# Optimization experiments

Measured on AMD Instinct MI355X. Metric: run time of the kernel, lower is better.

## Reference

```python
import jax, jax.numpy as jnp
import numpy as np
import math

B_SZ, T_LEN, DIM = 1, 1024, 1024
D_STATE, EXPAND, NUM_SCALES, CONV_K = 16, 2, 3, 4
D_INNER = EXPAND * DIM
EPS_LOG = 1e-38
LN_EPS = 1e-5


def _causal_dwconv(x, w, b):
    # x: (B,T,D), w: (D,1,K) depthwise, b: (D,). torch Conv1d(pad=K-1)[:, :, :T] == left-pad K-1 (causal).
    y = jax.lax.conv_general_dilated(
        jnp.transpose(x, (0, 2, 1)), w, window_strides=(1,),
        padding=[(CONV_K - 1, 0)], dimension_numbers=('NCH', 'OIH', 'NCH'),
        feature_group_count=w.shape[0])
    return jnp.transpose(y, (0, 2, 1)) + b


def _ssm_core(x, cw, cb, xw, dtw, dtb, Dp):
    # x: (B,T,d_inner)
    xc = jax.nn.silu(_causal_dwconv(x, cw, cb))
    proj = xc @ xw.T                               # (B,T,2*d_state)
    B_ssm, C_ssm = proj[..., :D_STATE], proj[..., D_STATE:]
    dt = jax.nn.softplus(B_ssm @ dtw.T + dtb)      # (B,T,d_inner)
    dt = jax.nn.softplus(dt)                       # selective_scan applies softplus a second time (faithful)
    A = -jnp.arange(1, D_STATE + 1, dtype=xc.dtype)  # (d_state,) == -A_init row, same for every d_inner channel
    dA = jnp.exp(dt[..., None] * A)                # (B,T,d_inner,d_state)
    dBx = dt[..., None] * B_ssm[:, :, None, :] * xc[..., None]
    log_dA = jnp.log(jnp.clip(dA, EPS_LOG))
    log_dBx = jnp.log(jnp.clip(dBx, EPS_LOG))
    # parallel_scan_cpu: h = exp(cumsum(log_dA) + logcumsumexp(log_dBx - cumsum(log_dA)))
    a_star = jnp.cumsum(log_dA, axis=1)
    h = jnp.exp(a_star + jax.lax.cumlogsumexp(log_dBx - a_star, axis=1))
    return jnp.einsum('bts,btds->btd', C_ssm, h) + Dp * xc


def _downsample(x, stride):
    if stride == 1:
        return x
    Bb, T, D = x.shape
    Tt = (T // stride) * stride
    return x[:, :Tt].reshape(Bb, Tt // stride, stride, D).mean(2)


def _upsample(x, T_out):
    # F.interpolate(mode='linear', align_corners=False)
    T_in = x.shape[1]
    if T_in == T_out:
        return x
    scale = T_in / T_out
    pos = jnp.clip((jnp.arange(T_out, dtype=jnp.float32) + 0.5) * scale - 0.5, 0.0, T_in - 1)
    lo = jnp.floor(pos).astype(jnp.int32)
    hi = jnp.minimum(lo + 1, T_in - 1)
    w = (pos - lo.astype(pos.dtype))[None, :, None]
    return x[:, lo] * (1.0 - w) + x[:, hi] * w


def _forward(x, in_proj_w, conv_w, conv_b, xproj_w, dtproj_w, dtproj_b,
             D_param, scale_weights, gate_w1, gate_w2, out_proj_w, ln_g, ln_b):
    residual = x
    xz = x @ in_proj_w.T                           # (B,T,2*d_inner)
    x_in, gate = xz[..., :D_INNER], xz[..., D_INNER:]
    outs = []
    for s in range(NUM_SCALES):
        x_s = _downsample(x_in, 2 ** s)
        y_s = _ssm_core(x_s, conv_w[s], conv_b[s], xproj_w[s], dtproj_w[s], dtproj_b[s], D_param[s])
        outs.append(_upsample(y_s, x.shape[1]))
    w = jax.nn.softmax(scale_weights)
    fused = sum(w[s] * outs[s] for s in range(NUM_SCALES))
    ctx = sum(outs) / NUM_SCALES
    gate_ctx = jax.nn.sigmoid(jax.nn.silu(ctx @ gate_w1.T) @ gate_w2.T)
    out = (fused * gate_ctx) * jax.nn.silu(gate)
    out = out @ out_proj_w.T
    y = out + residual
    mu = y.mean(-1, keepdims=True)
    var = ((y - mu) ** 2).mean(-1, keepdims=True)
    return (y - mu) / jnp.sqrt(var + LN_EPS) * ln_g + ln_b


def setup_inputs() -> dict:
    key = jax.random.key(0)
    ks = jax.random.split(key, 12)
    g = lambda k, shp, s: (jax.random.normal(k, shp, jnp.float32) * s)
    return {
        'x': g(ks[0], (B_SZ, T_LEN, DIM), 1.0),
        'in_proj_w': g(ks[1], (2 * D_INNER, DIM), DIM ** -0.5),
        'conv_w': g(ks[2], (NUM_SCALES, D_INNER, 1, CONV_K), CONV_K ** -0.5),
        'conv_b': g(ks[3], (NUM_SCALES, D_INNER), 0.02),
        'xproj_w': g(ks[4], (NUM_SCALES, 2 * D_STATE, D_INNER), D_INNER ** -0.5),
        'dtproj_w': g(ks[5], (NUM_SCALES, D_INNER, D_STATE), D_STATE ** -0.5),
        'dtproj_b': jax.random.uniform(ks[6], (NUM_SCALES, D_INNER), jnp.float32,
                                       math.log(0.001), math.log(0.1)),
        'D_param': jnp.ones((NUM_SCALES, D_INNER), jnp.float32),
        'scale_weights': jnp.ones((NUM_SCALES,), jnp.float32) / NUM_SCALES,
        'gate_w1': g(ks[7], (D_INNER // 2, D_INNER), D_INNER ** -0.5),
        'gate_w2': g(ks[8], (D_INNER, D_INNER // 2), (D_INNER // 2) ** -0.5),
        'out_proj_w': g(ks[9], (DIM, D_INNER), D_INNER ** -0.5),
        'ln_g': jnp.ones((DIM,), jnp.float32),
        'ln_b': jnp.zeros((DIM,), jnp.float32),
    }


def reference(x, in_proj_w, conv_w, conv_b, xproj_w, dtproj_w, dtproj_b,
              D_param, scale_weights, gate_w1, gate_w2, out_proj_w, ln_g, ln_b):
    return _forward(x, in_proj_w, conv_w, conv_b, xproj_w, dtproj_w, dtproj_b,
                    D_param, scale_weights, gate_w1, gate_w2, out_proj_w, ln_g, ln_b)
```

## Files before the change

kernel.cpp:

```cpp
#include <hip/hip_runtime.h>

typedef unsigned short u16;
typedef float floatx2 __attribute__((ext_vector_type(2)));
typedef float floatx4 __attribute__((ext_vector_type(4)));
typedef short shortx8 __attribute__((ext_vector_type(8)));

#define DIN 2048

__device__ __forceinline__ u16 f2bf(float f){
  unsigned u = __float_as_uint(f);
  u = (u + 0x7fffu + ((u>>16)&1u))>>16;
  return (u16)u;
}
__device__ __forceinline__ float sigf(float x){ return 1.f/(1.f+__expf(-x)); }
__device__ __forceinline__ float siluf(float x){ return x*sigf(x); }
__device__ __forceinline__ floatx2 max2(floatx2 a, floatx2 b){
  floatx2 r; r.x = fmaxf(a.x, b.x); r.y = fmaxf(a.y, b.y); return r;
}

#define OFF_WINP  0ull
#define OFF_WG1   8388608ull
#define OFF_WG2   12582912ull
#define OFF_WOP   16777216ull
#define OFF_XB    20971520ull
#define OFF_XIN   23068672ull
#define OFF_SGATE 31457280ull
#define OFF_X1    39845888ull
#define OFF_X2    44040192ull
#define OFF_XC0   46137344ull
#define OFF_XC1   54525952ull
#define OFF_FUSED 60817408ull
#define OFF_G3O   69206016ull
#define OFF_Y0    75497472ull
#define OFF_Y1    83886080ull
#define OFF_Y2    88080384ull
#define OFF_P0    90177536ull
#define OFF_P1    90308608ull
#define OFF_P2    90374144ull
#define OFF_HC    92274688ull
#define OFF_HINIT 121634816ull
#define OFF_SARR  136314880ull
#define OFF_CTXB  OFF_XC0
#define OFF_T1B   OFF_XC1
#define OFF_T1A0  OFF_XIN
#define OFF_T1A1  OFF_X1
#define OFF_YPA0  OFF_Y1
#define OFF_YPA1  (OFF_XC0 + 4194304ull)

__device__ __forceinline__ void gld_lds16(const void* g, void* l){
  __builtin_amdgcn_global_load_lds((const __attribute__((address_space(1))) unsigned*)g,
                                   (__attribute__((address_space(3))) unsigned*)l, 16, 0, 0);
}

__global__ __launch_bounds__(256) void cvt_kernel(
    const float* __restrict__ s0, u16* __restrict__ d0,
    const float* __restrict__ s1, u16* __restrict__ d1)
{
  int i = (blockIdx.x*256 + threadIdx.x)*4;
  const float* s; u16* d;
  if (i < 4194304){ s=s0; d=d0; }
  else            { s=s1; d=d1; i -= 4194304; }
  const float4 v = *(const float4*)(s + i);
  ushort4 o; o.x = f2bf(v.x); o.y = f2bf(v.y); o.z = f2bf(v.z); o.w = f2bf(v.w);
  *(ushort4*)(d + i) = o;
}

template<int MODE, int BM>
__global__ __launch_bounds__(256) void gemm_bt(
    const u16* __restrict__ A, const u16* __restrict__ B,
    int N, int K, int Ks,
    float* __restrict__ out_f, float* __restrict__ out_f2, u16* __restrict__ out_b,
    const float* __restrict__ ex0f, const float* __restrict__ ex1f,
    float* __restrict__ ex0, float* __restrict__ ex1)
{
  constexpr int NI = BM/32;
  constexpr int IP = BM/64;
  __shared__ u16 smA[2][BM*32];
  __shared__ u16 smB[2][BM*32];
  const int tid  = threadIdx.x;
  const int m0   = blockIdx.y * BM;
  const int n0   = blockIdx.x * BM;
  const int wv   = tid >> 6;
  const int lane = tid & 63;
  const int mw   = (wv >> 1) * (BM/2);
  const int nw   = (wv & 1) * (BM/2);
  const int quad = lane >> 4;
  const int l16  = lane & 15;
  const int srow = tid >> 2;
  const int scol = (tid & 3) * 8;

  floatx4 acc[NI][NI];
#pragma unroll
  for (int i=0;i<NI;i++)
#pragma unroll
    for (int j=0;j<NI;j++) acc[i][j] = (floatx4)0.f;

  const int kStart = blockIdx.z * Ks;
  const int kEnd   = kStart + Ks;

  auto stage = [&](int buf, int k0){
#pragma unroll
    for (int p=0;p<IP;p++){
      gld_lds16(A + (size_t)(m0 + p*64 + srow)*K + k0 + scol, &smA[buf][p*2048 + wv*512]);
      gld_lds16(B + (size_t)(n0 + p*64 + srow)*K + k0 + scol, &smB[buf][p*2048 + wv*512]);
    }
  };

  stage(0, kStart);
  int cur = 0;
  for (int k0 = kStart; k0 < kEnd; k0 += 32) {
    __syncthreads();
    if (k0 + 32 < kEnd) stage(cur^1, k0+32);
    shortx8 af[NI], bfr[NI];
#pragma unroll
    for (int i=0;i<NI;i++){
      af[i]  = *(const shortx8*)&smA[cur][(mw + i*16 + l16)*32 + quad*8];
      bfr[i] = *(const shortx8*)&smB[cur][(nw + i*16 + l16)*32 + quad*8];
    }
#pragma unroll
    for (int i=0;i<NI;i++)
#pragma unroll
      for (int j=0;j<NI;j++)
        acc[i][j] = __builtin_amdgcn_mfma_f32_16x16x32_bf16(af[i], bfr[j], acc[i][j], 0, 0, 0);
    cur ^= 1;
  }

#pragma unroll
  for (int i=0;i<NI;i++){
    const int mb = m0 + mw + i*16 + quad*4;
#pragma unroll
    for (int j=0;j<NI;j++){
      const int n = n0 + nw + j*16 + l16;
      const floatx4 v4 = acc[i][j];
      if (MODE == 0){
        if (n < 2048){
#pragma unroll
          for (int r=0;r<4;r++) out_f[(size_t)(mb+r)*2048 + n] = v4[r];
          ex0[(size_t)(mb>>1)*2048 + n]       = 0.5f*(v4[0]+v4[1]);
          ex0[(size_t)((mb>>1)+1)*2048 + n]   = 0.5f*(v4[2]+v4[3]);
          ex1[(size_t)(mb>>2)*2048 + n]       = 0.25f*(v4[0]+v4[1]+v4[2]+v4[3]);
        } else {
#pragma unroll
          for (int r=0;r<4;r++) out_f2[(size_t)(mb+r)*2048 + (n-2048)] = siluf(v4[r]);
        }
      } else if (MODE == 2){
#pragma unroll
        for (int r=0;r<4;r++){
          const size_t idx = (size_t)(mb+r)*N + n;
          out_b[idx] = f2bf(sigf(v4[r]) * ex0f[idx] * ex1f[idx]);
        }
      } else {
        float* dst = blockIdx.z ? out_f2 : out_f;
#pragma unroll
        for (int r=0;r<4;r++) dst[(size_t)(mb+r)*N + n] = v4[r];
      }
    }
  }
}

__global__ __launch_bounds__(256) void g2_epi(const float* __restrict__ a,
    const float* __restrict__ b, u16* __restrict__ o){
  const int i = (blockIdx.x*256 + threadIdx.x)*4;
  const float4 va = *(const float4*)(a+i);
  const float4 vb = *(const float4*)(b+i);
  ushort4 r;
  r.x = f2bf(siluf(va.x+vb.x)); r.y = f2bf(siluf(va.y+vb.y));
  r.z = f2bf(siluf(va.z+vb.z)); r.w = f2bf(siluf(va.w+vb.w));
  *(ushort4*)(o+i) = r;
}

__global__ __launch_bounds__(256) void xproj_kernel(const float* __restrict__ x0,
    const float* __restrict__ x1, const float* __restrict__ x2,
    const float* __restrict__ cw, const float* __restrict__ cb,
    const float* __restrict__ xw,
    float* __restrict__ p0, float* __restrict__ p1, float* __restrict__ p2,
    const float* __restrict__ gw1c, u16* __restrict__ wG1o,
    const float* __restrict__ gw2c, u16* __restrict__ wG2o,
    const float* __restrict__ opwc, u16* __restrict__ wOpo){
  __shared__ float srow[DIN];
  if (blockIdx.x >= 1792){
    int i = (int)(blockIdx.x - 1792)*1024 + threadIdx.x*4;
    const float* sp; u16* dp;
    if (i < 2097152)      { sp=gw1c; dp=wG1o; }
    else if (i < 4194304) { sp=gw2c; dp=wG2o; i-=2097152; }
    else                  { sp=opwc; dp=wOpo; i-=4194304; }
    const float4 v = *(const float4*)(sp + i);
    ushort4 o; o.x = f2bf(v.x); o.y = f2bf(v.y); o.z = f2bf(v.z); o.w = f2bf(v.w);
    *(ushort4*)(dp + i) = o;
    return;
  }
  const int b = blockIdx.x;
  const float* xs; float* proj; int s, t;
  if (b < 1024)      { s=0; t=b;       xs=x0; proj=p0; }
  else if (b < 1536) { s=1; t=b-1024;  xs=x1; proj=p1; }
  else               { s=2; t=b-1536;  xs=x2; proj=p2; }
  const int tid = threadIdx.x;
#pragma unroll
  for (int q=0;q<2;q++){
    const int k = (q*256 + tid)*4;
    float4 xv[4];
#pragma unroll
    for (int j=0;j<4;j++){
      const int tt = t - 3 + j;
      if (tt >= 0) xv[j] = *(const float4*)(xs + (size_t)tt*DIN + k);
      else { xv[j].x = 0.f; xv[j].y = 0.f; xv[j].z = 0.f; xv[j].w = 0.f; }
    }
    const float4 w0 = *(const float4*)(cw + ((size_t)(s*DIN) + k + 0)*4);
    const float4 w1 = *(const float4*)(cw + ((size_t)(s*DIN) + k + 1)*4);
    const float4 w2 = *(const float4*)(cw + ((size_t)(s*DIN) + k + 2)*4);
    const float4 w3 = *(const float4*)(cw + ((size_t)(s*DIN) + k + 3)*4);
    const float4 cb4 = *(const float4*)(cb + (size_t)(s*DIN) + k);
    float4 r;
    r.x = siluf(cb4.x + w0.x*xv[0].x + w0.y*xv[1].x + w0.z*xv[2].x + w0.w*xv[3].x);
    r.y = siluf(cb4.y + w1.x*xv[0].y + w1.y*xv[1].y + w1.z*xv[2].y + w1.w*xv[3].y);
    r.z = siluf(cb4.z + w2.x*xv[0].z + w2.y*xv[1].z + w2.z*xv[2].z + w2.w*xv[3].z);
    r.w = siluf(cb4.w + w3.x*xv[0].w + w3.y*xv[1].w + w3.z*xv[2].w + w3.w*xv[3].w);
    *(float4*)&srow[k] = r;
  }
  __syncthreads();
  const int i = tid >> 3;
  const int j = tid & 7;
  const float4* w4 = (const float4*)(xw + ((size_t)s*32 + i)*DIN);
  const float4* s4 = (const float4*)srow;
  float acc = 0.f;
#pragma unroll 8
  for (int c=0;c<64;c++){
    const float4 sv = s4[j + 8*c];
    const float4 wv = w4[j + 8*c];
    acc += sv.x*wv.x + sv.y*wv.y + sv.z*wv.z + sv.w*wv.w;
  }
  acc += __shfl_xor(acc,1); acc += __shfl_xor(acc,2); acc += __shfl_xor(acc,4);
  if (j == 0) proj[t*32 + i] = acc;
}

__global__ __launch_bounds__(128) void scan_p1(
    const float* __restrict__ x0, const float* __restrict__ x1, const float* __restrict__ x2,
    const float* __restrict__ p0, const float* __restrict__ p1, const float* __restrict__ p2,
    const float* __restrict__ cw, const float* __restrict__ cb,
    const float* __restrict__ dtw, const float* __restrict__ dtb,
    float* __restrict__ Sarr, float* __restrict__ Hc)
{
  __shared__ float sproj[16*32];
  int b = blockIdx.x;
  const float *xs, *proj; int base, s;
  if (b < 1024)      { xs=x0; proj=p0; base=0;  s=0; }
  else if (b < 1536) { b-=1024; xs=x1; proj=p1; base=64; s=1; }
  else               { b-=1536; xs=x2; proj=p2; base=96; s=2; }
  const int chunk = b >> 4;
  const int tid   = threadIdx.x;
  const int d     = (b & 15)*128 + tid;
  const int t0    = chunk*16;
  {
    const int k = tid*4;
    *(float4*)&sproj[k] = *(const float4*)&proj[t0*32 + k];
  }
  __syncthreads();

  const float4 wc  = *(const float4*)(cw + ((size_t)(s*DIN) + d)*4);
  const float  cbv = cb[s*DIN + d];
  floatx2 w2[8];
  const floatx2* wr = (const floatx2*)(dtw + ((size_t)(s*DIN) + d)*16);
#pragma unroll
  for (int k=0;k<8;k++) w2[k] = wr[k];
  const float bias = dtb[s*DIN + d];
  const floatx2 eps2 = {1e-38f, 1e-38f};

  floatx2 H2[8];
#pragma unroll
  for (int k=0;k<8;k++) H2[k] = (floatx2)0.f;
  float S = 0.f;
  const float* xp = xs + d;
  float h0=0.f, h1=0.f, h2=0.f;
  if (chunk){
    h0 = xp[(size_t)(t0-3)*DIN];
    h1 = xp[(size_t)(t0-2)*DIN];
    h2 = xp[(size_t)(t0-1)*DIN];
  }
  for (int tt=0; tt<16; tt++){
    const float xv  = xp[(size_t)(t0+tt)*DIN];
    const float xcv = siluf(cbv + wc.x*h0 + wc.y*h1 + wc.z*h2 + wc.w*xv);
    h0=h1; h1=h2; h2=xv;
    const floatx2* Bp2 = (const floatx2*)&sproj[tt*32];
    floatx2 zz = (floatx2)0.f;
#pragma unroll
    for (int k=0;k<8;k++) zz += Bp2[k]*w2[k];
    float z = fminf(zz.x + zz.y + bias, 60.f);
    const float E     = __expf(z);
    const float denom = 2.f + E;
    const float e     = __builtin_amdgcn_rcpf(denom);
    const float dtv   = __logf(denom);
    S += dtv;
    const floatx2 c2  = {dtv*xcv, dtv*xcv};
    const floatx2 es  = {e*e, e*e};
    floatx2 ep2 = {e, e*e};
#pragma unroll
    for (int k=0;k<8;k++){
      const floatx2 dA  = max2(ep2, eps2);
      const floatx2 dBx = max2(c2*Bp2[k], eps2);
      H2[k] = dA*H2[k] + dBx;
      ep2 *= es;
    }
  }
  Sarr[(size_t)(base+chunk)*2048 + d] = S;
  float* o = Hc + (size_t)(base+chunk)*32768 + d;
#pragma unroll
  for (int k=0;k<8;k++){
    o[(size_t)(2*k  )*2048] = H2[k].x;
    o[(size_t)(2*k+1)*2048] = H2[k].y;
  }
}

__global__ __launch_bounds__(256) void scan_combine(const float* __restrict__ Sarr,
    const float* __restrict__ Hc, float* __restrict__ Hinit){
  int id = blockIdx.x*256 + threadIdx.x;
  int base, C;
  if (id < 32768)      { base=0;  C=64; }
  else if (id < 65536) { id-=32768; base=64; C=32; }
  else                 { id-=65536; base=96; C=16; }
  const int n = id >> 11, d = id & 2047;
  const float fn = -(float)(n+1);
  const size_t off = (size_t)base*32768 + id;
  const float* hc = Hc + off;
  float* hi = Hinit + off;
  const float* sp = Sarr + (size_t)base*2048 + d;
  float H = 0.f;
  for (int c=0;c<C;c++){
    hi[(size_t)c*32768] = H;
    const float e = __expf(fn * sp[(size_t)c*2048]);
    H = e*H + hc[(size_t)c*32768];
  }
}

__global__ __launch_bounds__(128) void scan_p2(
    const float* __restrict__ x0, const float* __restrict__ x1, const float* __restrict__ x2,
    const float* __restrict__ p0, const float* __restrict__ p1, const float* __restrict__ p2,
    const float* __restrict__ cw, const float* __restrict__ cb,
    const float* __restrict__ dtw, const float* __restrict__ dtb,
    const float* __restrict__ Hinit, const float* __restrict__ Dp_all,
    float* __restrict__ y0, float* __restrict__ y1, float* __restrict__ y2)
{
  __shared__ float sproj[16*32];
  int b = blockIdx.x;
  const float *xs, *proj; float* y; int base, s;
  if (b < 1024)      { xs=x0; proj=p0; y=y0; base=0;  s=0; }
  else if (b < 1536) { b-=1024; xs=x1; proj=p1; y=y1; base=64; s=1; }
  else               { b-=1536; xs=x2; proj=p2; y=y2; base=96; s=2; }
  const int chunk = b >> 4;
  const int tid   = threadIdx.x;
  const int d     = (b & 15)*128 + tid;
  const int t0    = chunk*16;
  {
    const int k = tid*4;
    *(float4*)&sproj[k] = *(const float4*)&proj[t0*32 + k];
  }
  __syncthreads();

  const float4 wc  = *(const float4*)(cw + ((size_t)(s*DIN) + d)*4);
  const float  cbv = cb[s*DIN + d];
  floatx2 w2[8];
  const floatx2* wr = (const floatx2*)(dtw + ((size_t)(s*DIN) + d)*16);
#pragma unroll
  for (int k=0;k<8;k++) w2[k] = wr[k];
  const float bias = dtb[s*DIN + d];

  floatx2 H2[8];
  const float* hi = Hinit + (size_t)(base+chunk)*32768 + d;
#pragma unroll
  for (int k=0;k<8;k++){
    H2[k].x = hi[(size_t)(2*k  )*2048];
    H2[k].y = hi[(size_t)(2*k+1)*2048];
  }
  const float Dv = Dp_all[s*DIN + d];
  const floatx2 eps2 = {1e-38f, 1e-38f};
  const float* xp = xs + d;
  float* yp = y + (size_t)t0*DIN + d;
  float h0=0.f, h1=0.f, h2=0.f;
  if (chunk){
    h0 = xp[(size_t)(t0-3)*DIN];
    h1 = xp[(size_t)(t0-2)*DIN];
    h2 = xp[(size_t)(t0-1)*DIN];
  }
  for (int tt=0; tt<16; tt++){
    const float xv  = xp[(size_t)(t0+tt)*DIN];
    const float xcv = siluf(cbv + wc.x*h0 + wc.y*h1 + wc.z*h2 + wc.w*xv);
    h0=h1; h1=h2; h2=xv;
    const floatx2* Bp2 = (const floatx2*)&sproj[tt*32];
    floatx2 zz = (floatx2)0.f;
#pragma unroll
    for (int k=0;k<8;k++) zz += Bp2[k]*w2[k];
    float z = fminf(zz.x + zz.y + bias, 60.f);
    const float E     = __expf(z);
    const float denom = 2.f + E;
    const float e     = __builtin_amdgcn_rcpf(denom);
    const float dtv   = __logf(denom);
    const floatx2 c2 = {dtv*xcv, dtv*xcv};
    const floatx2 es = {e*e, e*e};
    floatx2 ep2 = {e, e*e};
    floatx2 pacc2 = (floatx2)0.f;
#pragma unroll
    for (int k=0;k<8;k++){
      const floatx2 dA  = max2(ep2, eps2);
      const floatx2 dBx = max2(c2*Bp2[k], eps2);
      H2[k] = dA*H2[k] + dBx;
      pacc2 += Bp2[8+k]*H2[k];
      ep2 *= es;
    }
    yp[(size_t)tt*DIN] = pacc2.x + pacc2.y + Dv*xcv;
  }
}

__device__ __forceinline__ float ups_read(const float* __restrict__ ys, int Tin, int t, int d){
  const float scale = (float)Tin * (1.f/1024.f);
  float pos = ((float)t + 0.5f)*scale - 0.5f;
  pos = fminf(fmaxf(pos, 0.f), (float)(Tin-1));
  const int lo = (int)floorf(pos);
  const float w = pos - (float)lo;
  const int hi = min(lo+1, Tin-1);
  return ys[(size_t)lo*DIN + d]*(1.f-w) + ys[(size_t)hi*DIN + d]*w;
}

__global__ __launch_bounds__(256) void fuse_kernel(const float* __restrict__ y0,
    const float* __restrict__ y1, const float* __restrict__ y2,
    const float* __restrict__ sw, u16* __restrict__ ctxb, float* __restrict__ fused){
  const int idx = blockIdx.x*256 + threadIdx.x;
  const int t = idx >> 11, d = idx & 2047;
  const float w0r = sw[0], w1r = sw[1], w2r = sw[2];
  const float mx = fmaxf(w0r, fmaxf(w1r, w2r));
  float e0 = __expf(w0r-mx), e1 = __expf(w1r-mx), e2 = __expf(w2r-mx);
  const float inv = 1.f/(e0+e1+e2);
  e0 *= inv; e1 *= inv; e2 *= inv;
  const float o0 = y0[idx];
  const float o1 = ups_read(y1, 512, t, d);
  const float o2 = ups_read(y2, 256, t, d);
  fused[idx] = e0*o0 + e1*o1 + e2*o2;
  ctxb[idx]  = f2bf((o0+o1+o2)*(1.f/3.f));
}

__global__ __launch_bounds__(256) void ln_kernel(const float* __restrict__ ya,
    const float* __restrict__ yb, const float* __restrict__ xr,
    const float* __restrict__ g, const float* __restrict__ b, float* __restrict__ out){
  __shared__ float red[4];
  const int t = blockIdx.x;
  const size_t ro = (size_t)t*1024;
  float v[4];
  float s = 0.f;
#pragma unroll
  for (int i=0;i<4;i++){
    const int c = threadIdx.x + i*256;
    v[i] = ya[ro+c] + yb[ro+c] + xr[ro+c];
    s += v[i];
  }
  s += __shfl_xor(s,1); s += __shfl_xor(s,2); s += __shfl_xor(s,4);
  s += __shfl_xor(s,8); s += __shfl_xor(s,16); s += __shfl_xor(s,32);
  if ((threadIdx.x & 63) == 0) red[threadIdx.x>>6] = s;
  __syncthreads();
  const float mu = (red[0]+red[1]+red[2]+red[3]) * (1.f/1024.f);
  __syncthreads();
  float q = 0.f;
#pragma unroll
  for (int i=0;i<4;i++){ const float dd = v[i]-mu; q += dd*dd; }
  q += __shfl_xor(q,1); q += __shfl_xor(q,2); q += __shfl_xor(q,4);
  q += __shfl_xor(q,8); q += __shfl_xor(q,16); q += __shfl_xor(q,32);
  if ((threadIdx.x & 63) == 0) red[threadIdx.x>>6] = q;
  __syncthreads();
  const float rstd = rsqrtf((red[0]+red[1]+red[2]+red[3]) * (1.f/1024.f) + 1e-5f);
#pragma unroll
  for (int i=0;i<4;i++){
    const int c = threadIdx.x + i*256;
    out[ro + c] = (v[i]-mu)*rstd*g[c] + b[c];
  }
}

extern "C" void kernel_launch(void* const* d_in, const int* in_sizes, int n_in,
                              void* d_out, int out_size, void* d_ws, size_t ws_size,
                              hipStream_t stream) {
  const float* x     = (const float*)d_in[0];
  const float* inpw  = (const float*)d_in[1];
  const float* convw = (const float*)d_in[2];
  const float* convb = (const float*)d_in[3];
  const float* xpw   = (const float*)d_in[4];
  const float* dtw   = (const float*)d_in[5];
  const float* dtb   = (const float*)d_in[6];
  const float* Dp    = (const float*)d_in[7];
  const float* sw    = (const float*)d_in[8];
  const float* gw1   = (const float*)d_in[9];
  const float* gw2   = (const float*)d_in[10];
  const float* opw   = (const float*)d_in[11];
  const float* lng   = (const float*)d_in[12];
  const float* lnb   = (const float*)d_in[13];
  float* out = (float*)d_out;

  char* ws = (char*)d_ws;
  u16*    wInp  = (u16*)   (ws + OFF_WINP);
  u16*    wG1   = (u16*)   (ws + OFF_WG1);
  u16*    wG2   = (u16*)   (ws + OFF_WG2);
  u16*    wOp   = (u16*)   (ws + OFF_WOP);
  u16*    xb    = (u16*)   (ws + OFF_XB);
  float*  xin   = (float*) (ws + OFF_XIN);
  float*  sgate = (float*) (ws + OFF_SGATE);
  float*  x1    = (float*) (ws + OFF_X1);
  float*  x2    = (float*) (ws + OFF_X2);
  float*  y0    = (float*) (ws + OFF_Y0);
  float*  y1    = (float*) (ws + OFF_Y1);
  float*  y2    = (float*) (ws + OFF_Y2);
  float*  p0    = (float*) (ws + OFF_P0);
  float*  p1    = (float*) (ws + OFF_P1);
  float*  p2    = (float*) (ws + OFF_P2);
  float*  Sarr  = (float*) (ws + OFF_SARR);
  float*  Hc    = (float*) (ws + OFF_HC);
  float*  Hinit = (float*) (ws + OFF_HINIT);
  u16*    ctxb  = (u16*)   (ws + OFF_CTXB);
  u16*    t1b   = (u16*)   (ws + OFF_T1B);
  float*  fused = (float*) (ws + OFF_FUSED);
  u16*    g3o   = (u16*)   (ws + OFF_G3O);
  float*  t1a0  = (float*) (ws + OFF_T1A0);
  float*  t1a1  = (float*) (ws + OFF_T1A1);
  float*  ypa0  = (float*) (ws + OFF_YPA0);
  float*  ypa1  = (float*) (ws + OFF_YPA1);

  cvt_kernel<<<5120, 256, 0, stream>>>(inpw, wInp, x, xb);
  gemm_bt<0,64><<<dim3(64, 16, 1), 256, 0, stream>>>(xb, wInp, 4096, 1024, 1024,
                                                     xin, sgate, nullptr, nullptr, nullptr, x1, x2);
  xproj_kernel<<<7936, 256, 0, stream>>>(xin, x1, x2, convw, convb, xpw, p0, p1, p2,
                                         gw1, wG1, gw2, wG2, opw, wOp);
  scan_p1<<<1792, 128, 0, stream>>>(xin, x1, x2, p0, p1, p2, convw, convb, dtw, dtb, Sarr, Hc);
  scan_combine<<<384, 256, 0, stream>>>(Sarr, Hc, Hinit);
  scan_p2<<<1792, 128, 0, stream>>>(xin, x1, x2, p0, p1, p2, convw, convb, dtw, dtb,
                                    Hinit, Dp, y0, y1, y2);
  fuse_kernel<<<(1024*DIN)/256, 256, 0, stream>>>(y0, y1, y2, sw, ctxb, fused);
  gemm_bt<4,64><<<dim3(16, 16, 2), 256, 0, stream>>>(ctxb, wG1, 1024, 2048, 1024,
                                                     t1a0, t1a1, nullptr, nullptr, nullptr, nullptr, nullptr);
  g2_epi<<<1024, 256, 0, stream>>>(t1a0, t1a1, t1b);
  gemm_bt<2,64><<<dim3(32, 16, 1), 256, 0, stream>>>(t1b, wG2, 2048, 1024, 1024,
                                                     nullptr, nullptr, g3o, fused, sgate, nullptr, nullptr);
  gemm_bt<4,64><<<dim3(16, 16, 2), 256, 0, stream>>>(g3o, wOp, 1024, 2048, 1024,
                                                     ypa0, ypa1, nullptr, nullptr, nullptr, nullptr, nullptr);
  ln_kernel<<<1024, 256, 0, stream>>>(ypa0, ypa1, x, lng, lnb, out);
}
```

Baseline: 280.3 us.

## Fuse scan passes, combine and scale fusion into one persistent kernel with grid barriers

```diff
diff --git a/kernel.cpp b/kernel.cpp
--- a/kernel.cpp
+++ b/kernel.cpp
@@ -40,6 +40,7 @@
 #define OFF_HC    92274688ull
 #define OFF_HINIT 121634816ull
 #define OFF_SARR  136314880ull
+#define OFF_BAR   137232384ull
 #define OFF_CTXB  OFF_XC0
 #define OFF_T1B   OFF_XC1
 #define OFF_T1A0  OFF_XIN
@@ -52,10 +53,23 @@
                                    (__attribute__((address_space(3))) unsigned*)l, 16, 0, 0);
 }
 
+__device__ __forceinline__ void gbar(unsigned* cnt, unsigned expected){
+  __syncthreads();
+  if (threadIdx.x == 0){
+    __threadfence();
+    atomicAdd(cnt, 1u);
+    while (atomicAdd(cnt, 0u) < expected) __builtin_amdgcn_s_sleep(16);
+    __threadfence();
+  }
+  __syncthreads();
+}
+
 __global__ __launch_bounds__(256) void cvt_kernel(
     const float* __restrict__ s0, u16* __restrict__ d0,
-    const float* __restrict__ s1, u16* __restrict__ d1)
+    const float* __restrict__ s1, u16* __restrict__ d1,
+    unsigned* __restrict__ bar)
 {
+  if (blockIdx.x == 0 && threadIdx.x < 4) bar[threadIdx.x] = 0u;
   int i = (blockIdx.x*256 + threadIdx.x)*4;
   const float* s; u16* d;
   if (i < 4194304){ s=s0; d=d0; }
@@ -233,182 +247,6 @@
   if (j == 0) proj[t*32 + i] = acc;
 }
 
-__global__ __launch_bounds__(128) void scan_p1(
-    const float* __restrict__ x0, const float* __restrict__ x1, const float* __restrict__ x2,
-    const float* __restrict__ p0, const float* __restrict__ p1, const float* __restrict__ p2,
-    const float* __restrict__ cw, const float* __restrict__ cb,
-    const float* __restrict__ dtw, const float* __restrict__ dtb,
-    float* __restrict__ Sarr, float* __restrict__ Hc)
-{
-  __shared__ float sproj[16*32];
-  int b = blockIdx.x;
-  const float *xs, *proj; int base, s;
-  if (b < 1024)      { xs=x0; proj=p0; base=0;  s=0; }
-  else if (b < 1536) { b-=1024; xs=x1; proj=p1; base=64; s=1; }
-  else               { b-=1536; xs=x2; proj=p2; base=96; s=2; }
-  const int chunk = b >> 4;
-  const int tid   = threadIdx.x;
-  const int d     = (b & 15)*128 + tid;
-  const int t0    = chunk*16;
-  {
-    const int k = tid*4;
-    *(float4*)&sproj[k] = *(const float4*)&proj[t0*32 + k];
-  }
-  __syncthreads();
-
-  const float4 wc  = *(const float4*)(cw + ((size_t)(s*DIN) + d)*4);
-  const float  cbv = cb[s*DIN + d];
-  floatx2 w2[8];
-  const floatx2* wr = (const floatx2*)(dtw + ((size_t)(s*DIN) + d)*16);
-#pragma unroll
-  for (int k=0;k<8;k++) w2[k] = wr[k];
-  const float bias = dtb[s*DIN + d];
-  const floatx2 eps2 = {1e-38f, 1e-38f};
-
-  floatx2 H2[8];
-#pragma unroll
-  for (int k=0;k<8;k++) H2[k] = (floatx2)0.f;
-  float S = 0.f;
-  const float* xp = xs + d;
-  float h0=0.f, h1=0.f, h2=0.f;
-  if (chunk){
-    h0 = xp[(size_t)(t0-3)*DIN];
-    h1 = xp[(size_t)(t0-2)*DIN];
-    h2 = xp[(size_t)(t0-1)*DIN];
-  }
-  for (int tt=0; tt<16; tt++){
-    const float xv  = xp[(size_t)(t0+tt)*DIN];
-    const float xcv = siluf(cbv + wc.x*h0 + wc.y*h1 + wc.z*h2 + wc.w*xv);
-    h0=h1; h1=h2; h2=xv;
-    const floatx2* Bp2 = (const floatx2*)&sproj[tt*32];
-    floatx2 zz = (floatx2)0.f;
-#pragma unroll
-    for (int k=0;k<8;k++) zz += Bp2[k]*w2[k];
-    float z = fminf(zz.x + zz.y + bias, 60.f);
-    const float E     = __expf(z);
-    const float denom = 2.f + E;
-    const float e     = __builtin_amdgcn_rcpf(denom);
-    const float dtv   = __logf(denom);
-    S += dtv;
-    const floatx2 c2  = {dtv*xcv, dtv*xcv};
-    const floatx2 es  = {e*e, e*e};
-    floatx2 ep2 = {e, e*e};
-#pragma unroll
-    for (int k=0;k<8;k++){
-      const floatx2 dA  = max2(ep2, eps2);
-      const floatx2 dBx = max2(c2*Bp2[k], eps2);
-      H2[k] = dA*H2[k] + dBx;
-      ep2 *= es;
-    }
-  }
-  Sarr[(size_t)(base+chunk)*2048 + d] = S;
-  float* o = Hc + (size_t)(base+chunk)*32768 + d;
-#pragma unroll
-  for (int k=0;k<8;k++){
-    o[(size_t)(2*k  )*2048] = H2[k].x;
-    o[(size_t)(2*k+1)*2048] = H2[k].y;
-  }
-}
-
-__global__ __launch_bounds__(256) void scan_combine(const float* __restrict__ Sarr,
-    const float* __restrict__ Hc, float* __restrict__ Hinit){
-  int id = blockIdx.x*256 + threadIdx.x;
-  int base, C;
-  if (id < 32768)      { base=0;  C=64; }
-  else if (id < 65536) { id-=32768; base=64; C=32; }
-  else                 { id-=65536; base=96; C=16; }
-  const int n = id >> 11, d = id & 2047;
-  const float fn = -(float)(n+1);
-  const size_t off = (size_t)base*32768 + id;
-  const float* hc = Hc + off;
-  float* hi = Hinit + off;
-  const float* sp = Sarr + (size_t)base*2048 + d;
-  float H = 0.f;
-  for (int c=0;c<C;c++){
-    hi[(size_t)c*32768] = H;
-    const float e = __expf(fn * sp[(size_t)c*2048]);
-    H = e*H + hc[(size_t)c*32768];
-  }
-}
-
-__global__ __launch_bounds__(128) void scan_p2(
-    const float* __restrict__ x0, const float* __restrict__ x1, const float* __restrict__ x2,
-    const float* __restrict__ p0, const float* __restrict__ p1, const float* __restrict__ p2,
-    const float* __restrict__ cw, const float* __restrict__ cb,
-    const float* __restrict__ dtw, const float* __restrict__ dtb,
-    const float* __restrict__ Hinit, const float* __restrict__ Dp_all,
-    float* __restrict__ y0, float* __restrict__ y1, float* __restrict__ y2)
-{
-  __shared__ float sproj[16*32];
-  int b = blockIdx.x;
-  const float *xs, *proj; float* y; int base, s;
-  if (b < 1024)      { xs=x0; proj=p0; y=y0; base=0;  s=0; }
-  else if (b < 1536) { b-=1024; xs=x1; proj=p1; y=y1; base=64; s=1; }
-  else               { b-=1536; xs=x2; proj=p2; y=y2; base=96; s=2; }
-  const int chunk = b >> 4;
-  const int tid   = threadIdx.x;
-  const int d     = (b & 15)*128 + tid;
-  const int t0    = chunk*16;
-  {
-    const int k = tid*4;
-    *(float4*)&sproj[k] = *(const float4*)&proj[t0*32 + k];
-  }
-  __syncthreads();
-
-  const float4 wc  = *(const float4*)(cw + ((size_t)(s*DIN) + d)*4);
-  const float  cbv = cb[s*DIN + d];
-  floatx2 w2[8];
-  const floatx2* wr = (const floatx2*)(dtw + ((size_t)(s*DIN) + d)*16);
-#pragma unroll
-  for (int k=0;k<8;k++) w2[k] = wr[k];
-  const float bias = dtb[s*DIN + d];
-
-  floatx2 H2[8];
-  const float* hi = Hinit + (size_t)(base+chunk)*32768 + d;
-#pragma unroll
-  for (int k=0;k<8;k++){
-    H2[k].x = hi[(size_t)(2*k  )*2048];
-    H2[k].y = hi[(size_t)(2*k+1)*2048];
-  }
-  const float Dv = Dp_all[s*DIN + d];
-  const floatx2 eps2 = {1e-38f, 1e-38f};
-  const float* xp = xs + d;
-  float* yp = y + (size_t)t0*DIN + d;
-  float h0=0.f, h1=0.f, h2=0.f;
-  if (chunk){
-    h0 = xp[(size_t)(t0-3)*DIN];
-    h1 = xp[(size_t)(t0-2)*DIN];
-    h2 = xp[(size_t)(t0-1)*DIN];
-  }
-  for (int tt=0; tt<16; tt++){
-    const float xv  = xp[(size_t)(t0+tt)*DIN];
-    const float xcv = siluf(cbv + wc.x*h0 + wc.y*h1 + wc.z*h2 + wc.w*xv);
-    h0=h1; h1=h2; h2=xv;
-    const floatx2* Bp2 = (const floatx2*)&sproj[tt*32];
-    floatx2 zz = (floatx2)0.f;
-#pragma unroll
-    for (int k=0;k<8;k++) zz += Bp2[k]*w2[k];
-    float z = fminf(zz.x + zz.y + bias, 60.f);
-    const float E     = __expf(z);
-    const float denom = 2.f + E;
-    const float e     = __builtin_amdgcn_rcpf(denom);
-    const float dtv   = __logf(denom);
-    const floatx2 c2 = {dtv*xcv, dtv*xcv};
-    const floatx2 es = {e*e, e*e};
-    floatx2 ep2 = {e, e*e};
-    floatx2 pacc2 = (floatx2)0.f;
-#pragma unroll
-    for (int k=0;k<8;k++){
-      const floatx2 dA  = max2(ep2, eps2);
-      const floatx2 dBx = max2(c2*Bp2[k], eps2);
-      H2[k] = dA*H2[k] + dBx;
-      pacc2 += Bp2[8+k]*H2[k];
-      ep2 *= es;
-    }
-    yp[(size_t)tt*DIN] = pacc2.x + pacc2.y + Dv*xcv;
-  }
-}
-
 __device__ __forceinline__ float ups_read(const float* __restrict__ ys, int Tin, int t, int d){
   const float scale = (float)Tin * (1.f/1024.f);
   float pos = ((float)t + 0.5f)*scale - 0.5f;
@@ -419,21 +257,166 @@
   return ys[(size_t)lo*DIN + d]*(1.f-w) + ys[(size_t)hi*DIN + d]*w;
 }
 
-__global__ __launch_bounds__(256) void fuse_kernel(const float* __restrict__ y0,
-    const float* __restrict__ y1, const float* __restrict__ y2,
-    const float* __restrict__ sw, u16* __restrict__ ctxb, float* __restrict__ fused){
-  const int idx = blockIdx.x*256 + threadIdx.x;
-  const int t = idx >> 11, d = idx & 2047;
-  const float w0r = sw[0], w1r = sw[1], w2r = sw[2];
-  const float mx = fmaxf(w0r, fmaxf(w1r, w2r));
-  float e0 = __expf(w0r-mx), e1 = __expf(w1r-mx), e2 = __expf(w2r-mx);
-  const float inv = 1.f/(e0+e1+e2);
-  e0 *= inv; e1 *= inv; e2 *= inv;
-  const float o0 = y0[idx];
-  const float o1 = ups_read(y1, 512, t, d);
-  const float o2 = ups_read(y2, 256, t, d);
-  fused[idx] = e0*o0 + e1*o1 + e2*o2;
-  ctxb[idx]  = f2bf((o0+o1+o2)*(1.f/3.f));
+__global__ __launch_bounds__(256, 4) void scan_fused(
+    const float* __restrict__ x0, const float* __restrict__ x1, const float* __restrict__ x2,
+    const float* __restrict__ p0, const float* __restrict__ p1, const float* __restrict__ p2,
+    const float* __restrict__ cw, const float* __restrict__ cb,
+    const float* __restrict__ dtw, const float* __restrict__ dtb,
+    const float* __restrict__ Dp_all, const float* __restrict__ sw,
+    float* __restrict__ Sarr, float* __restrict__ Hc, float* __restrict__ Hinit,
+    float* __restrict__ y0, float* __restrict__ y1, float* __restrict__ y2,
+    u16* __restrict__ ctxb, float* __restrict__ fusedo, unsigned* bar)
+{
+  __shared__ float sproj[16*32];
+  int b = blockIdx.x;
+  const float *xs, *proj; float* y; int base, s;
+  if (b < 512)      { xs=x0; proj=p0; y=y0; base=0;  s=0; }
+  else if (b < 768) { b-=512; xs=x1; proj=p1; y=y1; base=64; s=1; }
+  else              { b-=768; xs=x2; proj=p2; y=y2; base=96; s=2; }
+  const int chunk = b >> 3;
+  const int tid   = threadIdx.x;
+  const int d     = (b & 7)*256 + tid;
+  const int t0    = chunk*16;
+  {
+    const int k = tid*2;
+    *(float2*)&sproj[k] = *(const float2*)&proj[t0*32 + k];
+  }
+  __syncthreads();
+
+  const float4 wc  = *(const float4*)(cw + ((size_t)(s*DIN) + d)*4);
+  const float  cbv = cb[s*DIN + d];
+  floatx2 w2[8];
+  const floatx2* wr = (const floatx2*)(dtw + ((size_t)(s*DIN) + d)*16);
+#pragma unroll
+  for (int k=0;k<8;k++) w2[k] = wr[k];
+  const float bias = dtb[s*DIN + d];
+  const floatx2 eps2 = {1e-38f, 1e-38f};
+
+  floatx2 H2[8];
+#pragma unroll
+  for (int k=0;k<8;k++) H2[k] = (floatx2)0.f;
+  float S = 0.f;
+  float dt_s[16], xcv_s[16];
+  const float* xp = xs + d;
+  float h0=0.f, h1=0.f, h2=0.f;
+  if (chunk){
+    h0 = xp[(size_t)(t0-3)*DIN];
+    h1 = xp[(size_t)(t0-2)*DIN];
+    h2 = xp[(size_t)(t0-1)*DIN];
+  }
+#pragma unroll
+  for (int tt=0; tt<16; tt++){
+    const float xv  = xp[(size_t)(t0+tt)*DIN];
+    const float xcv = siluf(cbv + wc.x*h0 + wc.y*h1 + wc.z*h2 + wc.w*xv);
+    h0=h1; h1=h2; h2=xv;
+    const floatx2* Bp2 = (const floatx2*)&sproj[tt*32];
+    floatx2 zz = (floatx2)0.f;
+#pragma unroll
+    for (int k=0;k<8;k++) zz += Bp2[k]*w2[k];
+    float z = fminf(zz.x + zz.y + bias, 60.f);
+    const float E     = __expf(z);
+    const float denom = 2.f + E;
+    const float e     = __builtin_amdgcn_rcpf(denom);
+    const float dtv   = __logf(denom);
+    dt_s[tt]  = dtv;
+    xcv_s[tt] = xcv;
+    S += dtv;
+    const floatx2 c2  = {dtv*xcv, dtv*xcv};
+    const floatx2 es  = {e*e, e*e};
+    floatx2 ep2 = {e, e*e};
+#pragma unroll
+    for (int k=0;k<8;k++){
+      const floatx2 dA  = max2(ep2, eps2);
+      const floatx2 dBx = max2(c2*Bp2[k], eps2);
+      H2[k] = dA*H2[k] + dBx;
+      ep2 *= es;
+    }
+  }
+  Sarr[(size_t)(base+chunk)*2048 + d] = S;
+  {
+    float* o = Hc + (size_t)(base+chunk)*32768 + d;
+#pragma unroll
+    for (int k=0;k<8;k++){
+      o[(size_t)(2*k  )*2048] = H2[k].x;
+      o[(size_t)(2*k+1)*2048] = H2[k].y;
+    }
+  }
+
+  gbar(bar+0, 896);
+
+  {
+    int id = blockIdx.x*256 + tid;
+    if (id < 98304){
+      int base2, C;
+      if (id < 32768)      { base2=0;  C=64; }
+      else if (id < 65536) { id-=32768; base2=64; C=32; }
+      else                 { id-=65536; base2=96; C=16; }
+      const int n = id >> 11, dd = id & 2047;
+      const float fn = -(float)(n+1);
+      const size_t off = (size_t)base2*32768 + id;
+      const float* hc = Hc + off;
+      float* hi = Hinit + off;
+      const float* sp = Sarr + (size_t)base2*2048 + dd;
+      float H = 0.f;
+      for (int c=0;c<C;c++){
+        hi[(size_t)c*32768] = H;
+        const float e = __expf(fn * sp[(size_t)c*2048]);
+        H = e*H + hc[(size_t)c*32768];
+      }
+    }
+  }
+
+  gbar(bar+1, 896);
+
+  {
+    const float* hi = Hinit + (size_t)(base+chunk)*32768 + d;
+#pragma unroll
+    for (int k=0;k<8;k++){
+      H2[k].x = hi[(size_t)(2*k  )*2048];
+      H2[k].y = hi[(size_t)(2*k+1)*2048];
+    }
+  }
+  const float Dv = Dp_all[s*DIN + d];
+  float* yp = y + (size_t)t0*DIN + d;
+#pragma unroll
+  for (int tt=0; tt<16; tt++){
+    const float dtv = dt_s[tt];
+    const float xcv = xcv_s[tt];
+    const float e   = __expf(-dtv);
+    const floatx2* Bp2 = (const floatx2*)&sproj[tt*32];
+    const floatx2 c2 = {dtv*xcv, dtv*xcv};
+    const floatx2 es = {e*e, e*e};
+    floatx2 ep2 = {e, e*e};
+    floatx2 pacc2 = (floatx2)0.f;
+#pragma unroll
+    for (int k=0;k<8;k++){
+      const floatx2 dA  = max2(ep2, eps2);
+      const floatx2 dBx = max2(c2*Bp2[k], eps2);
+      H2[k] = dA*H2[k] + dBx;
+      pacc2 += Bp2[8+k]*H2[k];
+      ep2 *= es;
+    }
+    yp[(size_t)tt*DIN] = pacc2.x + pacc2.y + Dv*xcv;
+  }
+
+  gbar(bar+2, 896);
+
+  {
+    const float w0r = sw[0], w1r = sw[1], w2r = sw[2];
+    const float mx = fmaxf(w0r, fmaxf(w1r, w2r));
+    float e0 = __expf(w0r-mx), e1 = __expf(w1r-mx), e2 = __expf(w2r-mx);
+    const float inv = 1.f/(e0+e1+e2);
+    e0 *= inv; e1 *= inv; e2 *= inv;
+    const int gid = blockIdx.x*256 + tid;
+    for (int idx = gid; idx < 1024*2048; idx += 896*256){
+      const int t = idx >> 11, dd = idx & 2047;
+      const float o0 = y0[idx];
+      const float o1 = ups_read(y1, 512, t, dd);
+      const float o2 = ups_read(y2, 256, t, dd);
+      fusedo[idx] = e0*o0 + e1*o1 + e2*o2;
+      ctxb[idx]   = f2bf((o0+o1+o2)*(1.f/3.f));
+    }
+  }
 }
 
 __global__ __launch_bounds__(256) void ln_kernel(const float* __restrict__ ya,
@@ -491,43 +474,42 @@
   float* out = (float*)d_out;
 
   char* ws = (char*)d_ws;
-  u16*    wInp  = (u16*)   (ws + OFF_WINP);
-  u16*    wG1   = (u16*)   (ws + OFF_WG1);
-  u16*    wG2   = (u16*)   (ws + OFF_WG2);
-  u16*    wOp   = (u16*)   (ws + OFF_WOP);
-  u16*    xb    = (u16*)   (ws + OFF_XB);
-  float*  xin   = (float*) (ws + OFF_XIN);
-  float*  sgate = (float*) (ws + OFF_SGATE);
-  float*  x1    = (float*) (ws + OFF_X1);
-  float*  x2    = (float*) (ws + OFF_X2);
-  float*  y0    = (float*) (ws + OFF_Y0);
-  float*  y1    = (float*) (ws + OFF_Y1);
-  float*  y2    = (float*) (ws + OFF_Y2);
-  float*  p0    = (float*) (ws + OFF_P0);
-  float*  p1    = (float*) (ws + OFF_P1);
-  float*  p2    = (float*) (ws + OFF_P2);
-  float*  Sarr  = (float*) (ws + OFF_SARR);
-  float*  Hc    = (float*) (ws + OFF_HC);
-  float*  Hinit = (float*) (ws + OFF_HINIT);
-  u16*    ctxb  = (u16*)   (ws + OFF_CTXB);
-  u16*    t1b   = (u16*)   (ws + OFF_T1B);
-  float*  fused = (float*) (ws + OFF_FUSED);
-  u16*    g3o   = (u16*)   (ws + OFF_G3O);
-  float*  t1a0  = (float*) (ws + OFF_T1A0);
-  float*  t1a1  = (float*) (ws + OFF_T1A1);
-  float*  ypa0  = (float*) (ws + OFF_YPA0);
-  float*  ypa1  = (float*) (ws + OFF_YPA1);
-
-  cvt_kernel<<<5120, 256, 0, stream>>>(inpw, wInp, x, xb);
+  u16*      wInp  = (u16*)     (ws + OFF_WINP);
+  u16*      wG1   = (u16*)     (ws + OFF_WG1);
+  u16*      wG2   = (u16*)     (ws + OFF_WG2);
+  u16*      wOp   = (u16*)     (ws + OFF_WOP);
+  u16*      xb    = (u16*)     (ws + OFF_XB);
+  float*    xin   = (float*)   (ws + OFF_XIN);
+  float*    sgate = (float*)   (ws + OFF_SGATE);
+  float*    x1    = (float*)   (ws + OFF_X1);
+  float*    x2    = (float*)   (ws + OFF_X2);
+  float*    y0    = (float*)   (ws + OFF_Y0);
+  float*    y1    = (float*)   (ws + OFF_Y1);
+  float*    y2    = (float*)   (ws + OFF_Y2);
+  float*    p0    = (float*)   (ws + OFF_P0);
+  float*    p1    = (float*)   (ws + OFF_P1);
+  float*    p2    = (float*)   (ws + OFF_P2);
+  float*    Sarr  = (float*)   (ws + OFF_SARR);
+  float*    Hc    = (float*)   (ws + OFF_HC);
+  float*    Hinit = (float*)   (ws + OFF_HINIT);
+  u16*      ctxb  = (u16*)     (ws + OFF_CTXB);
+  u16*      t1b   = (u16*)     (ws + OFF_T1B);
+  float*    fused = (float*)   (ws + OFF_FUSED);
+  u16*      g3o   = (u16*)     (ws + OFF_G3O);
+  float*    t1a0  = (float*)   (ws + OFF_T1A0);
+  float*    t1a1  = (float*)   (ws + OFF_T1A1);
+  float*    ypa0  = (float*)   (ws + OFF_YPA0);
+  float*    ypa1  = (float*)   (ws + OFF_YPA1);
+  unsigned* bar   = (unsigned*)(ws + OFF_BAR);
+
+  cvt_kernel<<<5120, 256, 0, stream>>>(inpw, wInp, x, xb, bar);
   gemm_bt<0,64><<<dim3(64, 16, 1), 256, 0, stream>>>(xb, wInp, 4096, 1024, 1024,
                                                      xin, sgate, nullptr, nullptr, nullptr, x1, x2);
   xproj_kernel<<<7936, 256, 0, stream>>>(xin, x1, x2, convw, convb, xpw, p0, p1, p2,
                                          gw1, wG1, gw2, wG2, opw, wOp);
-  scan_p1<<<1792, 128, 0, stream>>>(xin, x1, x2, p0, p1, p2, convw, convb, dtw, dtb, Sarr, Hc);
-  scan_combine<<<384, 256, 0, stream>>>(Sarr, Hc, Hinit);
-  scan_p2<<<1792, 128, 0, stream>>>(xin, x1, x2, p0, p1, p2, convw, convb, dtw, dtb,
-                                    Hinit, Dp, y0, y1, y2);
-  fuse_kernel<<<(1024*DIN)/256, 256, 0, stream>>>(y0, y1, y2, sw, ctxb, fused);
+  scan_fused<<<896, 256, 0, stream>>>(xin, x1, x2, p0, p1, p2, convw, convb, dtw, dtb,
+                                      Dp, sw, Sarr, Hc, Hinit, y0, y1, y2,
+                                      ctxb, fused, bar);
   gemm_bt<4,64><<<dim3(16, 16, 2), 256, 0, stream>>>(ctxb, wG1, 1024, 2048, 1024,
                                                      t1a0, t1a1, nullptr, nullptr, nullptr, nullptr, nullptr);
   g2_epi<<<1024, 256, 0, stream>>>(t1a0, t1a1, t1b);
```

Result: slower. 553.8 us (+97.6%).
